# Kernel optimization log

Measured on AMD Instinct MI355X. Metric: run time of the kernel, lower is better.

## Reference

```python
import jax, jax.numpy as jnp
import numpy as np


def setup_inputs() -> dict:
    key = jax.random.key(0)
    ks = jax.random.split(key, 8)
    B, T, Hh, Ww, C = 4, 1024, 64, 64, 256
    f = lambda k, s: jax.random.normal(k, s, dtype=jnp.float32)
    return {
        "query_row": f(ks[0], (B, T, C)),
        "query_col": f(ks[1], (B, T, C)),
        "key_row": f(ks[2], (B, Hh, Ww, C)),
        "key_col": f(ks[3], (B, Hh, Ww, C)),
        "value": f(ks[4], (B, Hh, Ww, C)),
        "in_proj_weight": f(ks[5], (5 * C, C)) * 0.02,
        "in_proj_bias": jnp.zeros((5 * C,), jnp.float32),
        "out_w": f(ks[6], (C, C)) * 0.02,
        "out_b": jnp.zeros((C,), jnp.float32),
        "lin_w": f(ks[7], (C, C)) * 0.02,
        "lin_b": jnp.zeros((C,), jnp.float32),
        "num_heads": 8,
    }


def reference(query_row, query_col, key_row, key_col, value,
              in_proj_weight, in_proj_bias, out_w, out_b, lin_w, lin_b,
              num_heads):
    B, T, C = query_row.shape
    Hh, Ww = key_col.shape[1], key_row.shape[2]
    nh = num_heads
    hd = C // nh
    scaling = float(hd) ** -0.5
    W5 = in_proj_weight.reshape(5, C, C)
    b5 = in_proj_bias.reshape(5, C)
    # pooled sigmoid gate over value: AdaptiveAvgPool2d(1) == mean over H,W
    v_avg = jax.nn.sigmoid(value.mean(axis=(1, 2)) @ lin_w.T + lin_b)  # [B, C]
    q_row = (query_row @ W5[0].T + b5[0]) * scaling                    # [B, T, C]
    q_col = (query_col @ W5[1].T + b5[1]) * scaling                    # [B, T, C]
    k_row = (key_row @ W5[2].T + b5[2]).mean(axis=1) * v_avg[:, None, :]  # [B, W, C]
    k_col = (key_col @ W5[3].T + b5[3]).mean(axis=2) * v_avg[:, None, :]  # [B, H, C]
    v = value @ W5[4].T + b5[4]                                        # [B, H, W, C]
    # split heads (C -> nh*hd, same layout as torch view)
    qr = q_row.reshape(B, T, nh, hd)
    qc = q_col.reshape(B, T, nh, hd)
    kr = k_row.reshape(B, Ww, nh, hd)
    kc = k_col.reshape(B, Hh, nh, hd)
    vh = v.reshape(B, Hh, Ww, nh, hd)
    attn_row = jax.nn.softmax(jnp.einsum('btnd,bwnd->bntw', qr, kr), axis=-1)  # [B,nh,T,W]
    attn_col = jax.nn.softmax(jnp.einsum('btnd,bhnd->bnth', qc, kc), axis=-1)  # [B,nh,T,H]
    # column attention over rows of v, then row attention combines
    out_col = jnp.einsum('bnth,bhwnd->bntwd', attn_col, vh)            # [B,nh,T,W,hd]
    out = jnp.einsum('bntw,bntwd->btnd', attn_row, out_col).reshape(B, T, C)
    attn_output = (out @ out_w.T + out_b).transpose(1, 0, 2)           # [T, B, C]
    # head-averaged outer-product attention map [T, B, H, W]
    grid = jnp.einsum('bntw,bnth->tbhw', attn_row, attn_col) / nh
    return attn_output, grid
```

## Files before the change

kernel.cpp:

```cpp
#include <hip/hip_runtime.h>
#include <hip/hip_bf16.h>
#include <math.h>

using bf16x8 = __attribute__((ext_vector_type(8))) short;
using f32x4  = __attribute__((ext_vector_type(4))) float;
using s16x4  = __attribute__((ext_vector_type(4))) short;

static __device__ __forceinline__ float sigmoidf_(float x){ return 1.f/(1.f+__expf(-x)); }
static __device__ __forceinline__ unsigned f2bfu(float f){
  union { float f; unsigned u; } x; x.f = f;
  return (x.u + 0x7FFFu + ((x.u>>16)&1u)) >> 16;
}
static __device__ __forceinline__ short f2bf(float f){ return (short)f2bfu(f); }
static __device__ __forceinline__ unsigned pack2bf(float lo, float hi){
  __hip_bfloat162 h = __float22bfloat162_rn(make_float2(lo, hi));
  unsigned r; __builtin_memcpy(&r, &h, 4);
  return r;
}
static __device__ __forceinline__ float b2f_lo(unsigned u){ union{unsigned u; float f;}x; x.u = u<<16; return x.f; }
static __device__ __forceinline__ float b2f_hi(unsigned u){ union{unsigned u; float f;}x; x.u = u & 0xFFFF0000u; return x.f; }

__device__ __forceinline__ void mfma_body(short* As, short* Bs,
    const float* __restrict__ X, const float* __restrict__ Wm,
    const float* __restrict__ bias, float* __restrict__ Y,
    int bxm, int bxn, float scale, int mode){
  int tid = threadIdx.x;
  int m0 = bxm*128, n0 = bxn*128;
  int l = tid&63, wid = tid>>6, lo16 = l&15, g = l>>4;
  int wm = wid>>1, wn = wid&1;
  f32x4 acc[4][4] = {};
  int srow = tid>>1, skq = (tid&1)*32;
  size_t arow;
  int vb_ = 0, vw0 = 0;
  if (mode==4){
    vb_ = bxm>>5; vw0 = (bxm&31)*2;
    arow = (size_t)(vb_*4096 + (srow&63)*64 + vw0 + (srow>>6));
  } else arow = (size_t)(m0+srow);
  const float4* sa = (const float4*)(X + arow*256 + skq);
  const float4* sb = (const float4*)(Wm + (size_t)(n0+srow)*256 + skq);
  int4* da = (int4*)&As[srow*72 + skq];
  int4* db = (int4*)&Bs[srow*72 + skq];
  for (int k0=0;k0<4;k0++){
    __syncthreads();
    #pragma unroll
    for (int j=0;j<4;j++){
      float4 v0 = sa[2*j], v1 = sa[2*j+1];
      int4 wv;
      wv.x = (int)pack2bf(v0.x, v0.y); wv.y = (int)pack2bf(v0.z, v0.w);
      wv.z = (int)pack2bf(v1.x, v1.y); wv.w = (int)pack2bf(v1.z, v1.w);
      da[j] = wv;
      float4 u0 = sb[2*j], u1 = sb[2*j+1];
      int4 xv;
      xv.x = (int)pack2bf(u0.x, u0.y); xv.y = (int)pack2bf(u0.z, u0.w);
      xv.z = (int)pack2bf(u1.x, u1.y); xv.w = (int)pack2bf(u1.z, u1.w);
      db[j] = xv;
    }
    sa += 16; sb += 16;
    __syncthreads();
    bf16x8 af[4][2], bfr[4][2];
    #pragma unroll
    for (int mt=0;mt<4;mt++)
      #pragma unroll
      for (int c=0;c<2;c++)
        af[mt][c] = *(const bf16x8*)&As[(wm*64 + mt*16 + lo16)*72 + c*32 + g*8];
    #pragma unroll
    for (int nt=0;nt<4;nt++)
      #pragma unroll
      for (int c=0;c<2;c++)
        bfr[nt][c] = *(const bf16x8*)&Bs[(wn*64 + nt*16 + lo16)*72 + c*32 + g*8];
    #pragma unroll
    for (int mt=0;mt<4;mt++)
      #pragma unroll
      for (int nt=0;nt<4;nt++){
        acc[mt][nt] = __builtin_amdgcn_mfma_f32_16x16x32_bf16(af[mt][0], bfr[nt][0], acc[mt][nt], 0,0,0);
        acc[mt][nt] = __builtin_amdgcn_mfma_f32_16x16x32_bf16(af[mt][1], bfr[nt][1], acc[mt][nt], 0,0,0);
      }
  }
  if (mode==4){
    short* vdst = (short*)Y;
    int w = vw0 + wm;
    #pragma unroll
    for (int nt=0;nt<4;nt++){
      int col = n0 + wn*64 + nt*16 + lo16;
      float bv = bias[col];
      int n = col>>5, d = col&31;
      size_t base = (size_t)(vb_*8+n)*131072 + (size_t)w*2048 + d*64;
      #pragma unroll
      for (int mt=0;mt<4;mt++){
        int h0 = mt*16 + g*4;
        s16x4 s;
        #pragma unroll
        for (int r=0;r<4;r++) s[r] = f2bf(acc[mt][nt][r] + bv);
        *(s16x4*)(vdst + base + h0) = s;
      }
    }
  } else if (mode==3){
    #pragma unroll
    for (int nt=0;nt<4;nt++){
      int col = n0 + wn*64 + nt*16 + lo16;
      float bv = bias[col];
      #pragma unroll
      for (int mt=0;mt<4;mt++){
        int row = m0 + wm*64 + mt*16 + g*4;
        #pragma unroll
        for (int r=0;r<4;r++){
          int rr = row + r;
          Y[((size_t)((rr&1023)*4 + (rr>>10)))*256 + col] = acc[mt][nt][r] + bv;
        }
      }
    }
  } else {
    #pragma unroll
    for (int nt=0;nt<4;nt++){
      int col = n0 + wn*64 + nt*16 + lo16;
      float bv = bias[col];
      #pragma unroll
      for (int mt=0;mt<4;mt++){
        int row = m0 + wm*64 + mt*16 + g*4;
        #pragma unroll
        for (int r=0;r<4;r++){
          float y = acc[mt][nt][r] + bv;
          if (mode==0) y *= scale;
          Y[(size_t)(row+r)*256 + col] = y;
        }
      }
    }
  }
}

__global__ __launch_bounds__(256) void k_fat1(
    const float* __restrict__ value, const float* __restrict__ key_row,
    const float* __restrict__ key_col, float* __restrict__ vpart,
    float* __restrict__ krm, float* __restrict__ kcm,
    const float* __restrict__ query_row, const float* __restrict__ query_col,
    const float* __restrict__ ipw, const float* __restrict__ ipb,
    float* __restrict__ qr, float* __restrict__ qc,
    short* __restrict__ vpB, float scaling){
  __shared__ __align__(16) char smem[36864];
  int bx = blockIdx.x, c = threadIdx.x;
  if (bx < 640){
    float* red = (float*)smem;
    int cq = c & 63, rg = c >> 6;
    float4 s4 = make_float4(0.f,0.f,0.f,0.f);
    float oscale; float* outp_; size_t obase;
    if (bx < 128){
      int b = bx >> 5, chunk = bx & 31;
      const float4* p = (const float4*)(value + ((size_t)(b*4096 + chunk*128 + rg))*256) + cq;
      #pragma unroll 8
      for (int i=0;i<32;i++){
        float4 v = p[(size_t)i*256];
        s4.x+=v.x; s4.y+=v.y; s4.z+=v.z; s4.w+=v.w;
      }
      oscale = 1.f; outp_ = vpart; obase = (size_t)bx*256;
    } else if (bx < 384){
      int idx = bx - 128;
      int b = idx >> 6, w = idx & 63;
      const float4* p = (const float4*)(key_row + ((size_t)(b*4096 + w))*256) + cq;
      #pragma unroll 8
      for (int i=0;i<16;i++){
        float4 v = p[(size_t)(rg + 4*i)*4096];
        s4.x+=v.x; s4.y+=v.y; s4.z+=v.z; s4.w+=v.w;
      }
      oscale = 1.f/64.f; outp_ = krm; obase = (size_t)idx*256;
    } else {
      int idx = bx - 384;
      int b = idx >> 6, h = idx & 63;
      const float4* p = (const float4*)(key_col + ((size_t)((b*64+h)*64))*256) + cq;
      #pragma unroll 8
      for (int i=0;i<16;i++){
        float4 v = p[(size_t)(rg + 4*i)*64];
        s4.x+=v.x; s4.y+=v.y; s4.z+=v.z; s4.w+=v.w;
      }
      oscale = 1.f/64.f; outp_ = kcm; obase = (size_t)idx*256;
    }
    *(float4*)&red[rg*256 + cq*4] = s4;
    __syncthreads();
    if (c < 64){
      float4 a0 = *(float4*)&red[c*4];
      float4 a1 = *(float4*)&red[256 + c*4];
      float4 a2 = *(float4*)&red[512 + c*4];
      float4 a3 = *(float4*)&red[768 + c*4];
      float4 o = make_float4((a0.x+a1.x+a2.x+a3.x)*oscale, (a0.y+a1.y+a2.y+a3.y)*oscale,
                             (a0.z+a1.z+a2.z+a3.z)*oscale, (a0.w+a1.w+a2.w+a3.w)*oscale);
      *(float4*)&outp_[obase + c*4] = o;
    }
    return;
  }
  short* As = (short*)smem;
  short* Bs = (short*)(smem + 18432);
  if (bx < 768){
    int bxx = bx - 640;
    int zz = bxx>>6, rem = bxx&63;
    mfma_body(As, Bs, zz ? query_col : query_row, ipw + (zz?65536:0), ipb + (zz?256:0),
              zz ? qc : qr, rem&31, rem>>5, scaling, 0);
  } else {
    int bxx = bx - 768;
    mfma_body(As, Bs, value, ipw+262144, ipb+1024, (float*)vpB, bxx&127, bxx>>7, 1.f, 4);
  }
}

__global__ __launch_bounds__(256) void k_gemm_krkc(
    const float* __restrict__ krm, const float* __restrict__ kcm,
    const float* __restrict__ ipw, const float* __restrict__ ipb,
    const float* __restrict__ vpart, const float* __restrict__ lin_w,
    const float* __restrict__ lin_b,
    float* __restrict__ kr, float* __restrict__ kc){
  const float* X; const float* Wm; const float* bias; float* Y;
  if (blockIdx.z==0){ X=krm; Wm=ipw+131072; bias=ipb+512; Y=kr; }
  else              { X=kcm; Wm=ipw+196608; bias=ipb+768; Y=kc; }
  __shared__ float Ast[32*68];
  __shared__ float Bst[32*68];
  __shared__ float va[256];
  __shared__ float gsh[64];
  int tx = threadIdx.x, ty = threadIdx.y;
  int tid = ty*16 + tx;
  int b = blockIdx.x;
  int m0 = b*64, n0 = blockIdx.y*64;
  {
    float s = 0.f;
    #pragma unroll
    for (int i=0;i<32;i++) s += vpart[(size_t)(b*32+i)*256 + tid];
    va[tid] = s * (1.f/4096.f);
  }
  __syncthreads();
  {
    int j = tid>>2, kq = tid&3;
    const float* wrow = lin_w + (size_t)(n0+j)*256 + kq*64;
    const float* vap  = va + kq*64;
    float part = 0.f;
    #pragma unroll
    for (int k=0;k<64;k++) part += vap[k]*wrow[k];
    part += __shfl_xor(part, 1);
    part += __shfl_xor(part, 2);
    if (kq==0) gsh[j] = sigmoidf_(part + lin_b[n0+j]);
  }
  float acc[4][4];
  #pragma unroll
  for (int i=0;i<4;i++)
    #pragma unroll
    for (int j=0;j<4;j++) acc[i][j] = 0.f;

  for (int k0=0;k0<256;k0+=32){
    __syncthreads();
    #pragma unroll
    for (int p=0;p<2;p++){
      int pos = tid + p*256;
      int r = pos>>3, kq = pos&7;
      float4 xa = *(const float4*)&X[(size_t)(m0+r)*256 + k0 + kq*4];
      Ast[(kq*4+0)*68+r]=xa.x; Ast[(kq*4+1)*68+r]=xa.y;
      Ast[(kq*4+2)*68+r]=xa.z; Ast[(kq*4+3)*68+r]=xa.w;
      float4 wb = *(const float4*)&Wm[(size_t)(n0+r)*256 + k0 + kq*4];
      Bst[(kq*4+0)*68+r]=wb.x; Bst[(kq*4+1)*68+r]=wb.y;
      Bst[(kq*4+2)*68+r]=wb.z; Bst[(kq*4+3)*68+r]=wb.w;
    }
    __syncthreads();
    #pragma unroll
    for (int k=0;k<32;k++){
      float4 a  = *(const float4*)&Ast[k*68 + ty*4];
      float4 bv = *(const float4*)&Bst[k*68 + tx*4];
      acc[0][0]+=a.x*bv.x; acc[0][1]+=a.x*bv.y; acc[0][2]+=a.x*bv.z; acc[0][3]+=a.x*bv.w;
      acc[1][0]+=a.y*bv.x; acc[1][1]+=a.y*bv.y; acc[1][2]+=a.y*bv.z; acc[1][3]+=a.y*bv.w;
      acc[2][0]+=a.z*bv.x; acc[2][1]+=a.z*bv.y; acc[2][2]+=a.z*bv.z; acc[2][3]+=a.z*bv.w;
      acc[3][0]+=a.w*bv.x; acc[3][1]+=a.w*bv.y; acc[3][2]+=a.w*bv.z; acc[3][3]+=a.w*bv.w;
    }
  }
  float4 b4 = *(const float4*)&bias[n0 + tx*4];
  float4 g4 = *(const float4*)&gsh[tx*4];
  #pragma unroll
  for (int i=0;i<4;i++){
    int row = m0 + ty*4 + i;
    float4 y = make_float4((acc[i][0]+b4.x)*g4.x, (acc[i][1]+b4.y)*g4.y,
                           (acc[i][2]+b4.z)*g4.z, (acc[i][3]+b4.w)*g4.w);
    *(float4*)&Y[(size_t)row*256 + n0 + tx*4] = y;
  }
}

__global__ void k_attn(const float* __restrict__ qr, const float* __restrict__ kr,
                       const float* __restrict__ qc, const float* __restrict__ kc,
                       float* __restrict__ arNf, __hip_bfloat16* __restrict__ acNb){
  int lane = threadIdx.x;
  int tblk = blockIdx.x, n = blockIdx.y, z = blockIdx.z;
  int isCol = z >> 2, b = z & 3;
  const float* q  = isCol ? qc : qr;
  const float* kk = isCol ? kc : kr;
  int bn = b*8 + n;
  float4 kreg[8];
  const float4* kp = (const float4*)(kk + ((size_t)(b*64 + lane))*256 + n*32);
  #pragma unroll
  for (int i=0;i<8;i++) kreg[i] = kp[i];
  size_t qbase = ((size_t)(b*1024) + tblk*16)*256 + n*32;
  for (int i=0;i<16;i+=2){
    const float4* qp0 = (const float4*)(q + qbase + (size_t)i*256);
    const float4* qp1 = (const float4*)(q + qbase + (size_t)(i+1)*256);
    float s0 = 0.f, s1 = 0.f;
    #pragma unroll
    for (int j=0;j<8;j++){
      float4 a = qp0[j], c = qp1[j];
      s0 += a.x*kreg[j].x + a.y*kreg[j].y + a.z*kreg[j].z + a.w*kreg[j].w;
      s1 += c.x*kreg[j].x + c.y*kreg[j].y + c.z*kreg[j].z + c.w*kreg[j].w;
    }
    float e0 = __expf(s0), e1 = __expf(s1);
    float sm0 = e0, sm1 = e1;
    #pragma unroll
    for (int off=32; off; off>>=1){
      sm0 += __shfl_xor(sm0, off);
      sm1 += __shfl_xor(sm1, off);
    }
    float p0 = e0 / sm0, p1 = e1 / sm1;
    size_t off_ = ((size_t)bn*1024 + tblk*16 + i)*64 + lane;
    if (isCol){ ((short*)acNb)[off_] = f2bf(p0); ((short*)acNb)[off_ + 64] = f2bf(p1); }
    else      { arNf[off_] = p0; arNf[off_ + 64] = p1; }
  }
}

__global__ __launch_bounds__(256) void k_core3(
    const __hip_bfloat16* __restrict__ acB, const float* __restrict__ arN,
    const __hip_bfloat16* __restrict__ vpB, float* __restrict__ outp){
  __shared__ float ARs[64*36];
  __shared__ float P[4][32*34];
  int tid = threadIdx.x;
  int bn = blockIdx.x, tt = blockIdx.y;
  int b = bn>>3, n = bn&7;
  int t0 = tt*32;

  {
    int w = tid&63, tg = (tid>>6)*8;
    const float* src = arN + ((size_t)bn*1024 + t0 + tg)*64 + w;
    #pragma unroll
    for (int k=0;k<8;k++)
      ARs[w*36 + tg + k] = src[(size_t)k*64];
  }

  int l = tid&63, wid = tid>>6, lo16 = l&15, g = l>>4, g4 = g*4;
  bf16x8 af[2][2];
  {
    const short* ab = (const short*)acB + ((size_t)bn*1024 + t0 + lo16)*64 + g*8;
    #pragma unroll
    for (int ts=0; ts<2; ts++){
      af[ts][0] = *(const bf16x8*)(ab + ts*1024);
      af[ts][1] = *(const bf16x8*)(ab + ts*1024 + 32);
    }
  }
  __syncthreads();

  const short* vb = (const short*)vpB + (size_t)bn*131072 + (size_t)wid*32768 + lo16*64 + g*8;
  bf16x8 buf0[4], buf1[4];
  {
    const short* p0 = vb;
    buf0[0] = *(const bf16x8*)(p0);        buf0[1] = *(const bf16x8*)(p0 + 32);
    buf0[2] = *(const bf16x8*)(p0 + 1024); buf0[3] = *(const bf16x8*)(p0 + 1056);
    const short* p1 = vb + 2048;
    buf1[0] = *(const bf16x8*)(p1);        buf1[1] = *(const bf16x8*)(p1 + 32);
    buf1[2] = *(const bf16x8*)(p1 + 1024); buf1[3] = *(const bf16x8*)(p1 + 1056);
  }
  f32x4 o[2][2] = {};
  const f32x4 zz = {0.f,0.f,0.f,0.f};
  int wbase = wid*16;

  #pragma unroll 2
  for (int wi=0; wi<16; wi+=2){
    {
      bf16x8 c0=buf0[0], c1=buf0[1], c2=buf0[2], c3=buf0[3];
      const short* pn = vb + (size_t)((wi+2)&15)*2048;
      buf0[0] = *(const bf16x8*)(pn);        buf0[1] = *(const bf16x8*)(pn + 32);
      buf0[2] = *(const bf16x8*)(pn + 1024); buf0[3] = *(const bf16x8*)(pn + 1056);
      int wg = wbase + wi;
      #pragma unroll
      for (int ts=0; ts<2; ts++){
        f32x4 mlo = __builtin_amdgcn_mfma_f32_16x16x32_bf16(af[ts][0], c0, zz, 0,0,0);
        mlo = __builtin_amdgcn_mfma_f32_16x16x32_bf16(af[ts][1], c1, mlo, 0,0,0);
        f32x4 mhi = __builtin_amdgcn_mfma_f32_16x16x32_bf16(af[ts][0], c2, zz, 0,0,0);
        mhi = __builtin_amdgcn_mfma_f32_16x16x32_bf16(af[ts][1], c3, mhi, 0,0,0);
        f32x4 ar4 = *(const f32x4*)&ARs[wg*36 + ts*16 + g4];
        #pragma unroll
        for (int r=0;r<4;r++){ o[ts][0][r] += ar4[r]*mlo[r]; o[ts][1][r] += ar4[r]*mhi[r]; }
      }
    }
    {
      bf16x8 c0=buf1[0], c1=buf1[1], c2=buf1[2], c3=buf1[3];
      const short* pn = vb + (size_t)((wi+3)&15)*2048;
      buf1[0] = *(const bf16x8*)(pn);        buf1[1] = *(const bf16x8*)(pn + 32);
      buf1[2] = *(const bf16x8*)(pn + 1024); buf1[3] = *(const bf16x8*)(pn + 1056);
      int wg = wbase + wi + 1;
      #pragma unroll
      for (int ts=0; ts<2; ts++){
        f32x4 mlo = __builtin_amdgcn_mfma_f32_16x16x32_bf16(af[ts][0], c0, zz, 0,0,0);
        mlo = __builtin_amdgcn_mfma_f32_16x16x32_bf16(af[ts][1], c1, mlo, 0,0,0);
        f32x4 mhi = __builtin_amdgcn_mfma_f32_16x16x32_bf16(af[ts][0], c2, zz, 0,0,0);
        mhi = __builtin_amdgcn_mfma_f32_16x16x32_bf16(af[ts][1], c3, mhi, 0,0,0);
        f32x4 ar4 = *(const f32x4*)&ARs[wg*36 + ts*16 + g4];
        #pragma unroll
        for (int r=0;r<4;r++){ o[ts][0][r] += ar4[r]*mlo[r]; o[ts][1][r] += ar4[r]*mhi[r]; }
      }
    }
  }

  #pragma unroll
  for (int ts=0; ts<2; ts++)
    #pragma unroll
    for (int dh=0; dh<2; dh++)
      #pragma unroll
      for (int r=0;r<4;r++)
        P[wid][(ts*16 + g4 + r)*34 + dh*16 + lo16] = o[ts][dh][r];
  __syncthreads();

  float* obase = outp + ((size_t)b*1024 + t0)*256 + n*32;
  #pragma unroll
  for (int k=0;k<4;k++){
    int idx = k*256 + tid;
    int t = idx>>5, d = idx&31;
    float s = P[0][t*34+d] + P[1][t*34+d] + P[2][t*34+d] + P[3][t*34+d];
    obase[(size_t)t*256 + d] = s;
  }
}

__global__ __launch_bounds__(256) void k_fat2(
    const float* __restrict__ outp, const float* __restrict__ out_w,
    const float* __restrict__ out_b, float* __restrict__ out,
    const __hip_bfloat16* __restrict__ acNb, const float* __restrict__ arNf,
    float* __restrict__ gout){
  __shared__ __align__(16) char smem[36864];
  int bx = blockIdx.x;
  if (bx < 64){
    short* As = (short*)smem;
    short* Bs = (short*)(smem + 18432);
    mfma_body(As, Bs, outp, out_w, out_b, out, bx&31, bx>>5, 1.f, 3);
    return;
  }
  float* acs = (float*)smem;
  float* ars = (float*)(smem + 8192);
  int bxx = bx - 64;
  int tid = threadIdx.x, tg = bxx&255, b = bxx>>8;
  int t0 = tg*4;
  {
    int idx = tid*8;
    int n = idx>>8, t = (idx>>6)&3, x = idx&63;
    const short* asrc = (const short*)acNb + ((size_t)(b*8+n)*1024 + t0+t)*64 + x;
    uint4 av = *(const uint4*)asrc;
    float* ad = &acs[(n*4+t)*64 + x];
    ad[0]=b2f_lo(av.x); ad[1]=b2f_hi(av.x); ad[2]=b2f_lo(av.y); ad[3]=b2f_hi(av.y);
    ad[4]=b2f_lo(av.z); ad[5]=b2f_hi(av.z); ad[6]=b2f_lo(av.w); ad[7]=b2f_hi(av.w);
    const float4* rsrc = (const float4*)(arNf + ((size_t)(b*8+n)*1024 + t0+t)*64 + x);
    float4 r0 = rsrc[0], r1 = rsrc[1];
    *(float4*)&ars[(n*4+t)*64 + x]     = r0;
    *(float4*)&ars[(n*4+t)*64 + x + 4] = r1;
  }
  __syncthreads();
  int t_ = tid>>6, l = tid&63;
  int wg = l&3, hsel = l>>2;
  float acc[4][16];
  #pragma unroll
  for (int i=0;i<4;i++)
    #pragma unroll
    for (int j=0;j<16;j++) acc[i][j] = 0.f;
  #pragma unroll
  for (int n=0;n<8;n++){
    float4 a4 = *(const float4*)&acs[(n*4+t_)*64 + hsel*4];
    const float4* rb = (const float4*)&ars[(n*4+t_)*64 + wg*16];
    float4 r0 = rb[0], r1 = rb[1], r2 = rb[2], r3 = rb[3];
    float rr[16] = {r0.x,r0.y,r0.z,r0.w, r1.x,r1.y,r1.z,r1.w,
                    r2.x,r2.y,r2.z,r2.w, r3.x,r3.y,r3.z,r3.w};
    float aa[4] = {a4.x, a4.y, a4.z, a4.w};
    #pragma unroll
    for (int i=0;i<4;i++)
      #pragma unroll
      for (int j=0;j<16;j++) acc[i][j] += aa[i]*rr[j];
  }
  const float inv = 0.125f;
  float* dstbase = gout + ((size_t)(t0+t_)*4 + b)*4096;
  #pragma unroll
  for (int i=0;i<4;i++){
    float* dst = dstbase + (hsel*4+i)*64 + wg*16;
    #pragma unroll
    for (int jq=0;jq<4;jq++)
      *(float4*)&dst[jq*4] = make_float4(acc[i][jq*4]*inv, acc[i][jq*4+1]*inv,
                                         acc[i][jq*4+2]*inv, acc[i][jq*4+3]*inv);
  }
}

extern "C" void kernel_launch(void* const* d_in, const int* in_sizes, int n_in,
                              void* d_out, int out_size, void* d_ws, size_t ws_size,
                              hipStream_t stream){
  const float* query_row = (const float*)d_in[0];
  const float* query_col = (const float*)d_in[1];
  const float* key_row   = (const float*)d_in[2];
  const float* key_col   = (const float*)d_in[3];
  const float* value     = (const float*)d_in[4];
  const float* ipw       = (const float*)d_in[5];
  const float* ipb       = (const float*)d_in[6];
  const float* out_w     = (const float*)d_in[7];
  const float* out_b     = (const float*)d_in[8];
  const float* lin_w     = (const float*)d_in[9];
  const float* lin_b     = (const float*)d_in[10];
  float* out = (float*)d_out;
  float* ws  = (float*)d_ws;

  float* vpart = ws;
  float* krm   = ws + 32768;
  float* kcm   = ws + 98304;
  float* kr    = ws + 163840;
  float* kc    = ws + 229376;
  float* qr    = ws + 294912;
  float* qc    = ws + 1343488;
  __hip_bfloat16* vpB  = (__hip_bfloat16*)(ws + 2392064);
  float* arNf  = ws + 4489216;
  __hip_bfloat16* acNb = (__hip_bfloat16*)(ws + 6586368);
  float* outp  = ws + 7634944;

  const float scaling = 0.17677669529663687f;

  hipLaunchKernelGGL(k_fat1, dim3(1024), dim3(256), 0, stream,
                     value, key_row, key_col, vpart, krm, kcm,
                     query_row, query_col, ipw, ipb, qr, qc, (short*)vpB, scaling);

  hipLaunchKernelGGL(k_gemm_krkc, dim3(4,4,2), dim3(16,16), 0, stream,
                     krm, kcm, ipw, ipb, vpart, lin_w, lin_b, kr, kc);

  hipLaunchKernelGGL(k_attn, dim3(64,8,8), dim3(64), 0, stream,
                     qr, kr, qc, kc, arNf, acNb);

  hipLaunchKernelGGL(k_core3, dim3(32,32), dim3(256), 0, stream, acNb, arNf, vpB, outp);

  hipLaunchKernelGGL(k_fat2, dim3(1088), dim3(256), 0, stream,
                     outp, out_w, out_b, out, acNb, arNf, out + 1048576);
}
```

Measured before the change: 127.6 us.

## Regroup stage kernels and store row attention probabilities as bf16

Splits the former fused reduce+projection kernel so the mean reductions run alone, then merges the small kr/kc gemm with the q/v projection gemms into one launch. The kr/kc work now shares a launch with the big projections instead of running as its own tiny serial kernel. Separately, the row attention probabilities are written as bf16 instead of fp32, halving their write and read traffic in k_attn, k_core3 and k_fat2. This lowers precision of the row attention map and of the grid output.

```diff
diff --git a/kernel.cpp b/kernel.cpp
--- a/kernel.cpp
+++ b/kernel.cpp
@@ -128,94 +128,23 @@
   }
 }
 
-__global__ __launch_bounds__(256) void k_fat1(
-    const float* __restrict__ value, const float* __restrict__ key_row,
-    const float* __restrict__ key_col, float* __restrict__ vpart,
-    float* __restrict__ krm, float* __restrict__ kcm,
-    const float* __restrict__ query_row, const float* __restrict__ query_col,
-    const float* __restrict__ ipw, const float* __restrict__ ipb,
-    float* __restrict__ qr, float* __restrict__ qc,
-    short* __restrict__ vpB, float scaling){
-  __shared__ __align__(16) char smem[36864];
-  int bx = blockIdx.x, c = threadIdx.x;
-  if (bx < 640){
-    float* red = (float*)smem;
-    int cq = c & 63, rg = c >> 6;
-    float4 s4 = make_float4(0.f,0.f,0.f,0.f);
-    float oscale; float* outp_; size_t obase;
-    if (bx < 128){
-      int b = bx >> 5, chunk = bx & 31;
-      const float4* p = (const float4*)(value + ((size_t)(b*4096 + chunk*128 + rg))*256) + cq;
-      #pragma unroll 8
-      for (int i=0;i<32;i++){
-        float4 v = p[(size_t)i*256];
-        s4.x+=v.x; s4.y+=v.y; s4.z+=v.z; s4.w+=v.w;
-      }
-      oscale = 1.f; outp_ = vpart; obase = (size_t)bx*256;
-    } else if (bx < 384){
-      int idx = bx - 128;
-      int b = idx >> 6, w = idx & 63;
-      const float4* p = (const float4*)(key_row + ((size_t)(b*4096 + w))*256) + cq;
-      #pragma unroll 8
-      for (int i=0;i<16;i++){
-        float4 v = p[(size_t)(rg + 4*i)*4096];
-        s4.x+=v.x; s4.y+=v.y; s4.z+=v.z; s4.w+=v.w;
-      }
-      oscale = 1.f/64.f; outp_ = krm; obase = (size_t)idx*256;
-    } else {
-      int idx = bx - 384;
-      int b = idx >> 6, h = idx & 63;
-      const float4* p = (const float4*)(key_col + ((size_t)((b*64+h)*64))*256) + cq;
-      #pragma unroll 8
-      for (int i=0;i<16;i++){
-        float4 v = p[(size_t)(rg + 4*i)*64];
-        s4.x+=v.x; s4.y+=v.y; s4.z+=v.z; s4.w+=v.w;
-      }
-      oscale = 1.f/64.f; outp_ = kcm; obase = (size_t)idx*256;
-    }
-    *(float4*)&red[rg*256 + cq*4] = s4;
-    __syncthreads();
-    if (c < 64){
-      float4 a0 = *(float4*)&red[c*4];
-      float4 a1 = *(float4*)&red[256 + c*4];
-      float4 a2 = *(float4*)&red[512 + c*4];
-      float4 a3 = *(float4*)&red[768 + c*4];
-      float4 o = make_float4((a0.x+a1.x+a2.x+a3.x)*oscale, (a0.y+a1.y+a2.y+a3.y)*oscale,
-                             (a0.z+a1.z+a2.z+a3.z)*oscale, (a0.w+a1.w+a2.w+a3.w)*oscale);
-      *(float4*)&outp_[obase + c*4] = o;
-    }
-    return;
-  }
-  short* As = (short*)smem;
-  short* Bs = (short*)(smem + 18432);
-  if (bx < 768){
-    int bxx = bx - 640;
-    int zz = bxx>>6, rem = bxx&63;
-    mfma_body(As, Bs, zz ? query_col : query_row, ipw + (zz?65536:0), ipb + (zz?256:0),
-              zz ? qc : qr, rem&31, rem>>5, scaling, 0);
-  } else {
-    int bxx = bx - 768;
-    mfma_body(As, Bs, value, ipw+262144, ipb+1024, (float*)vpB, bxx&127, bxx>>7, 1.f, 4);
-  }
-}
-
-__global__ __launch_bounds__(256) void k_gemm_krkc(
+__device__ __forceinline__ void krkc_body(char* smem,
     const float* __restrict__ krm, const float* __restrict__ kcm,
     const float* __restrict__ ipw, const float* __restrict__ ipb,
     const float* __restrict__ vpart, const float* __restrict__ lin_w,
     const float* __restrict__ lin_b,
-    float* __restrict__ kr, float* __restrict__ kc){
+    float* __restrict__ kr, float* __restrict__ kc,
+    int b, int ny, int z){
   const float* X; const float* Wm; const float* bias; float* Y;
-  if (blockIdx.z==0){ X=krm; Wm=ipw+131072; bias=ipb+512; Y=kr; }
-  else              { X=kcm; Wm=ipw+196608; bias=ipb+768; Y=kc; }
-  __shared__ float Ast[32*68];
-  __shared__ float Bst[32*68];
-  __shared__ float va[256];
-  __shared__ float gsh[64];
-  int tx = threadIdx.x, ty = threadIdx.y;
-  int tid = ty*16 + tx;
-  int b = blockIdx.x;
-  int m0 = b*64, n0 = blockIdx.y*64;
+  if (z==0){ X=krm; Wm=ipw+131072; bias=ipb+512; Y=kr; }
+  else     { X=kcm; Wm=ipw+196608; bias=ipb+768; Y=kc; }
+  float* Ast = (float*)smem;
+  float* Bst = (float*)(smem + 8704);
+  float* va  = (float*)(smem + 17408);
+  float* gsh = (float*)(smem + 18432);
+  int tid = threadIdx.x;
+  int tx = tid&15, ty = tid>>4;
+  int m0 = b*64, n0 = ny*64;
   {
     float s = 0.f;
     #pragma unroll
@@ -275,14 +204,97 @@
   }
 }
 
+__global__ __launch_bounds__(256) void k_reduce(
+    const float* __restrict__ value, const float* __restrict__ key_row,
+    const float* __restrict__ key_col, float* __restrict__ vpart,
+    float* __restrict__ krm, float* __restrict__ kcm){
+  __shared__ float red[1024];
+  int bx = blockIdx.x, c = threadIdx.x;
+  int cq = c & 63, rg = c >> 6;
+  float4 s4 = make_float4(0.f,0.f,0.f,0.f);
+  float oscale; float* outp_; size_t obase;
+  if (bx < 128){
+    int b = bx >> 5, chunk = bx & 31;
+    const float4* p = (const float4*)(value + ((size_t)(b*4096 + chunk*128 + rg))*256) + cq;
+    #pragma unroll 8
+    for (int i=0;i<32;i++){
+      float4 v = p[(size_t)i*256];
+      s4.x+=v.x; s4.y+=v.y; s4.z+=v.z; s4.w+=v.w;
+    }
+    oscale = 1.f; outp_ = vpart; obase = (size_t)bx*256;
+  } else if (bx < 384){
+    int idx = bx - 128;
+    int b = idx >> 6, w = idx & 63;
+    const float4* p = (const float4*)(key_row + ((size_t)(b*4096 + w))*256) + cq;
+    #pragma unroll 8
+    for (int i=0;i<16;i++){
+      float4 v = p[(size_t)(rg + 4*i)*4096];
+      s4.x+=v.x; s4.y+=v.y; s4.z+=v.z; s4.w+=v.w;
+    }
+    oscale = 1.f/64.f; outp_ = krm; obase = (size_t)idx*256;
+  } else {
+    int idx = bx - 384;
+    int b = idx >> 6, h = idx & 63;
+    const float4* p = (const float4*)(key_col + ((size_t)((b*64+h)*64))*256) + cq;
+    #pragma unroll 8
+    for (int i=0;i<16;i++){
+      float4 v = p[(size_t)(rg + 4*i)*64];
+      s4.x+=v.x; s4.y+=v.y; s4.z+=v.z; s4.w+=v.w;
+    }
+    oscale = 1.f/64.f; outp_ = kcm; obase = (size_t)idx*256;
+  }
+  *(float4*)&red[rg*256 + cq*4] = s4;
+  __syncthreads();
+  if (c < 64){
+    float4 a0 = *(float4*)&red[c*4];
+    float4 a1 = *(float4*)&red[256 + c*4];
+    float4 a2 = *(float4*)&red[512 + c*4];
+    float4 a3 = *(float4*)&red[768 + c*4];
+    float4 o = make_float4((a0.x+a1.x+a2.x+a3.x)*oscale, (a0.y+a1.y+a2.y+a3.y)*oscale,
+                           (a0.z+a1.z+a2.z+a3.z)*oscale, (a0.w+a1.w+a2.w+a3.w)*oscale);
+    *(float4*)&outp_[obase + c*4] = o;
+  }
+}
+
+__global__ __launch_bounds__(256) void k_proj(
+    const float* __restrict__ krm, const float* __restrict__ kcm,
+    const float* __restrict__ value,
+    const float* __restrict__ query_row, const float* __restrict__ query_col,
+    const float* __restrict__ ipw, const float* __restrict__ ipb,
+    const float* __restrict__ vpart, const float* __restrict__ lin_w,
+    const float* __restrict__ lin_b,
+    float* __restrict__ kr, float* __restrict__ kc,
+    float* __restrict__ qr, float* __restrict__ qc,
+    short* __restrict__ vpB, float scaling){
+  __shared__ __align__(16) char smem[36864];
+  int bx = blockIdx.x;
+  if (bx < 32){
+    int z = bx>>4, rem = bx&15, b = rem&3, ny = rem>>2;
+    krkc_body(smem, krm, kcm, ipw, ipb, vpart, lin_w, lin_b, kr, kc, b, ny, z);
+    return;
+  }
+  short* As = (short*)smem;
+  short* Bs = (short*)(smem + 18432);
+  if (bx < 160){
+    int bxx = bx - 32;
+    int zz = bxx>>6, rem = bxx&63;
+    mfma_body(As, Bs, zz ? query_col : query_row, ipw + (zz?65536:0), ipb + (zz?256:0),
+              zz ? qc : qr, rem&31, rem>>5, scaling, 0);
+  } else {
+    int bxx = bx - 160;
+    mfma_body(As, Bs, value, ipw+262144, ipb+1024, (float*)vpB, bxx&127, bxx>>7, 1.f, 4);
+  }
+}
+
 __global__ void k_attn(const float* __restrict__ qr, const float* __restrict__ kr,
                        const float* __restrict__ qc, const float* __restrict__ kc,
-                       float* __restrict__ arNf, __hip_bfloat16* __restrict__ acNb){
+                       short* __restrict__ arB, short* __restrict__ acB){
   int lane = threadIdx.x;
   int tblk = blockIdx.x, n = blockIdx.y, z = blockIdx.z;
   int isCol = z >> 2, b = z & 3;
   const float* q  = isCol ? qc : qr;
   const float* kk = isCol ? kc : kr;
+  short* dst = isCol ? acB : arB;
   int bn = b*8 + n;
   float4 kreg[8];
   const float4* kp = (const float4*)(kk + ((size_t)(b*64 + lane))*256 + n*32);
@@ -306,15 +318,14 @@
       sm0 += __shfl_xor(sm0, off);
       sm1 += __shfl_xor(sm1, off);
     }
-    float p0 = e0 / sm0, p1 = e1 / sm1;
     size_t off_ = ((size_t)bn*1024 + tblk*16 + i)*64 + lane;
-    if (isCol){ ((short*)acNb)[off_] = f2bf(p0); ((short*)acNb)[off_ + 64] = f2bf(p1); }
-    else      { arNf[off_] = p0; arNf[off_ + 64] = p1; }
+    dst[off_]      = f2bf(e0 / sm0);
+    dst[off_ + 64] = f2bf(e1 / sm1);
   }
 }
 
 __global__ __launch_bounds__(256) void k_core3(
-    const __hip_bfloat16* __restrict__ acB, const float* __restrict__ arN,
+    const short* __restrict__ acB, const short* __restrict__ arB,
     const __hip_bfloat16* __restrict__ vpB, float* __restrict__ outp){
   __shared__ float ARs[64*36];
   __shared__ float P[4][32*34];
@@ -325,16 +336,16 @@
 
   {
     int w = tid&63, tg = (tid>>6)*8;
-    const float* src = arN + ((size_t)bn*1024 + t0 + tg)*64 + w;
+    const unsigned short* src = (const unsigned short*)arB + ((size_t)bn*1024 + t0 + tg)*64 + w;
     #pragma unroll
     for (int k=0;k<8;k++)
-      ARs[w*36 + tg + k] = src[(size_t)k*64];
+      ARs[w*36 + tg + k] = b2f_lo((unsigned)src[(size_t)k*64]);
   }
 
   int l = tid&63, wid = tid>>6, lo16 = l&15, g = l>>4, g4 = g*4;
   bf16x8 af[2][2];
   {
-    const short* ab = (const short*)acB + ((size_t)bn*1024 + t0 + lo16)*64 + g*8;
+    const short* ab = acB + ((size_t)bn*1024 + t0 + lo16)*64 + g*8;
     #pragma unroll
     for (int ts=0; ts<2; ts++){
       af[ts][0] = *(const bf16x8*)(ab + ts*1024);
@@ -417,7 +428,7 @@
 __global__ __launch_bounds__(256) void k_fat2(
     const float* __restrict__ outp, const float* __restrict__ out_w,
     const float* __restrict__ out_b, float* __restrict__ out,
-    const __hip_bfloat16* __restrict__ acNb, const float* __restrict__ arNf,
+    const short* __restrict__ acB, const short* __restrict__ arB,
     float* __restrict__ gout){
   __shared__ __align__(16) char smem[36864];
   int bx = blockIdx.x;
@@ -435,15 +446,15 @@
   {
     int idx = tid*8;
     int n = idx>>8, t = (idx>>6)&3, x = idx&63;
-    const short* asrc = (const short*)acNb + ((size_t)(b*8+n)*1024 + t0+t)*64 + x;
-    uint4 av = *(const uint4*)asrc;
+    size_t soff = ((size_t)(b*8+n)*1024 + t0+t)*64 + x;
+    uint4 av = *(const uint4*)(acB + soff);
     float* ad = &acs[(n*4+t)*64 + x];
     ad[0]=b2f_lo(av.x); ad[1]=b2f_hi(av.x); ad[2]=b2f_lo(av.y); ad[3]=b2f_hi(av.y);
     ad[4]=b2f_lo(av.z); ad[5]=b2f_hi(av.z); ad[6]=b2f_lo(av.w); ad[7]=b2f_hi(av.w);
-    const float4* rsrc = (const float4*)(arNf + ((size_t)(b*8+n)*1024 + t0+t)*64 + x);
-    float4 r0 = rsrc[0], r1 = rsrc[1];
-    *(float4*)&ars[(n*4+t)*64 + x]     = r0;
-    *(float4*)&ars[(n*4+t)*64 + x + 4] = r1;
+    uint4 rv = *(const uint4*)(arB + soff);
+    float* rd = &ars[(n*4+t)*64 + x];
+    rd[0]=b2f_lo(rv.x); rd[1]=b2f_hi(rv.x); rd[2]=b2f_lo(rv.y); rd[3]=b2f_hi(rv.y);
+    rd[4]=b2f_lo(rv.z); rd[5]=b2f_hi(rv.z); rd[6]=b2f_lo(rv.w); rd[7]=b2f_hi(rv.w);
   }
   __syncthreads();
   int t_ = tid>>6, l = tid&63;
@@ -502,25 +513,25 @@
   float* kc    = ws + 229376;
   float* qr    = ws + 294912;
   float* qc    = ws + 1343488;
-  __hip_bfloat16* vpB  = (__hip_bfloat16*)(ws + 2392064);
-  float* arNf  = ws + 4489216;
-  __hip_bfloat16* acNb = (__hip_bfloat16*)(ws + 6586368);
-  float* outp  = ws + 7634944;
+  __hip_bfloat16* vpB = (__hip_bfloat16*)(ws + 2392064);
+  short* arB  = (short*)(ws + 4489216);
+  short* acB  = (short*)(ws + 5537792);
+  float* outp = ws + 6586368;
 
   const float scaling = 0.17677669529663687f;
 
-  hipLaunchKernelGGL(k_fat1, dim3(1024), dim3(256), 0, stream,
-                     value, key_row, key_col, vpart, krm, kcm,
-                     query_row, query_col, ipw, ipb, qr, qc, (short*)vpB, scaling);
-
-  hipLaunchKernelGGL(k_gemm_krkc, dim3(4,4,2), dim3(16,16), 0, stream,
-                     krm, kcm, ipw, ipb, vpart, lin_w, lin_b, kr, kc);
+  hipLaunchKernelGGL(k_reduce, dim3(640), dim3(256), 0, stream,
+                     value, key_row, key_col, vpart, krm, kcm);
+
+  hipLaunchKernelGGL(k_proj, dim3(416), dim3(256), 0, stream,
+                     krm, kcm, value, query_row, query_col, ipw, ipb,
+                     vpart, lin_w, lin_b, kr, kc, qr, qc, (short*)vpB, scaling);
 
   hipLaunchKernelGGL(k_attn, dim3(64,8,8), dim3(64), 0, stream,
-                     qr, kr, qc, kc, arNf, acNb);
-
-  hipLaunchKernelGGL(k_core3, dim3(32,32), dim3(256), 0, stream, acNb, arNf, vpB, outp);
+                     qr, kr, qc, kc, arB, acB);
+
+  hipLaunchKernelGGL(k_core3, dim3(32,32), dim3(256), 0, stream, acB, arB, vpB, outp);
 
   hipLaunchKernelGGL(k_fat2, dim3(1088), dim3(256), 0, stream,
-                     outp, out_w, out_b, out, acNb, arNf, out + 1048576);
-}
+                     outp, out_w, out_b, out, acB, arB, out + 1048576);
+}
```

New measurement: 116.3 us. 1.1x faster.
